# Kernel tuning notes

Hardware: AMD Instinct MI355X
Metric: run time of the kernel (lower is better)

Reference implementation:

```python
import jax, jax.numpy as jnp
import numpy as np

N_USERS = 100000
N_ENTITIES = 150000
N_RELATIONS = 10
CHANNEL = 64
N_KG_EDGES = 1000000
N_UI_EDGES = 1000000
N_HOPS = 2


def setup_inputs() -> dict:
    key = jax.random.key(0)
    ks = jax.random.split(key, 9)
    user_emb = jax.random.normal(ks[0], (N_USERS, CHANNEL), dtype=jnp.float32)
    entity_emb = jax.random.normal(ks[1], (N_ENTITIES, CHANNEL), dtype=jnp.float32)
    edge_index = jax.random.randint(ks[2], (2, N_KG_EDGES), 0, N_ENTITIES, dtype=jnp.int32)
    # edge_type in [1, n_relations) as in the repo (relation 0 is the interact relation)
    edge_type = jax.random.randint(ks[3], (N_KG_EDGES,), 1, N_RELATIONS, dtype=jnp.int32)
    ui_u = jax.random.randint(ks[4], (N_UI_EDGES,), 0, N_USERS, dtype=jnp.int32)
    ui_i = jax.random.randint(ks[5], (N_UI_EDGES,), 0, N_ENTITIES, dtype=jnp.int32)
    inter_edge = jnp.stack([ui_u, ui_i], axis=0)
    inter_edge_w = jax.random.uniform(ks[6], (N_UI_EDGES,), dtype=jnp.float32)
    # learned params (xavier_uniform)
    def xavier(k, shape):
        fan_in, fan_out = shape[0], shape[1]
        a = float(np.sqrt(6.0 / (fan_in + fan_out)))
        return jax.random.uniform(k, shape, dtype=jnp.float32, minval=-a, maxval=a)
    relation_emb = xavier(ks[7], (N_RELATIONS, CHANNEL))
    W_Q = xavier(ks[8], (CHANNEL, CHANNEL))
    W_UI = xavier(jax.random.fold_in(key, 123), (CHANNEL, CHANNEL))
    return {
        'user_emb': user_emb, 'entity_emb': entity_emb,
        'edge_index': edge_index, 'edge_type': edge_type,
        'inter_edge': inter_edge, 'inter_edge_w': inter_edge_w,
        'relation_emb': relation_emb, 'W_Q': W_Q, 'W_UI': W_UI,
    }


def _segment_softmax(score, idx, num_segments):
    # scatter_softmax: stable softmax over edges sharing the same destination index
    m = jax.ops.segment_max(score, idx, num_segments=num_segments)
    m = jnp.where(jnp.isfinite(m), m, 0.0)  # empty segments -> -inf guard
    e = jnp.exp(score - jax.lax.stop_gradient(m)[idx])
    s = jax.ops.segment_sum(e, idx, num_segments=num_segments)
    return e / (s[idx] + 1e-16)


def _l2_normalize(x):
    # F.normalize(x) with default p=2, dim=1, eps=1e-12
    n = jnp.sqrt(jnp.sum(x * x, axis=1, keepdims=True))
    return x / jnp.maximum(n, 1e-12)


def _shared_layer_agg(user_emb, entity_emb, edge_index, edge_type,
                      inter_edge, inter_edge_w, relation_emb, W_Q, W_UI):
    n_entities = entity_emb.shape[0]
    n_users = user_emb.shape[0]
    head, tail = edge_index[0], edge_index[1]
    rel = relation_emb[edge_type - 1]              # [E, C]
    query = (entity_emb[head] @ W_Q) * rel          # [E, C]
    key = (entity_emb[tail] @ W_Q) * rel            # [E, C]
    edge_attn_score = jnp.sum(query + key, axis=-1)  # [E]
    value = entity_emb[tail] * rel                  # [E, C]
    attn = _segment_softmax(edge_attn_score, head, n_entities)
    entity_agg = jax.ops.segment_sum(value * attn[:, None], head, num_segments=n_entities)
    # user-item attention; note: original code reassigns relation_emb to the per-edge
    # gathered array, so relation_emb[-1] is the relation emb of the LAST KG edge.
    rel_last = rel[-1]                              # [C]
    u_idx, i_idx = inter_edge[0], inter_edge[1]
    quary_u = (user_emb[u_idx] @ W_UI) * rel_last   # [Eui, C]
    key_i = (entity_emb[i_idx] @ W_UI) * rel_last   # [Eui, C]
    score_ui = jnp.sum(quary_u + key_i, axis=-1)
    attn_ui = _segment_softmax(score_ui, u_idx, n_users)
    item_agg = inter_edge_w[:, None] * entity_emb[i_idx] * attn_ui[:, None]
    user_agg = jax.ops.segment_sum(item_agg, u_idx, num_segments=n_users)
    return entity_agg, user_agg


def reference(user_emb, entity_emb, edge_index, edge_type, inter_edge,
              inter_edge_w, relation_emb, W_Q, W_UI):
    entity_res_emb = entity_emb
    user_res_emb = user_emb
    for _ in range(N_HOPS):
        entity_emb, user_emb = _shared_layer_agg(
            user_emb, entity_emb, edge_index, edge_type,
            inter_edge, inter_edge_w, relation_emb, W_Q, W_UI)
        # mess_dropout disabled for deterministic reference (eval mode)
        entity_emb = _l2_normalize(entity_emb)
        user_emb = _l2_normalize(user_emb)
        entity_res_emb = entity_res_emb + entity_emb
        user_res_emb = user_res_emb + user_emb
    return entity_res_emb, user_res_emb
```

## Files before the change

kernel.cpp:

```cpp
#include <hip/hip_runtime.h>


__device__ __forceinline__ float red16(float p) {
    p += __shfl_xor(p, 1, 64);
    p += __shfl_xor(p, 2, 64);
    p += __shfl_xor(p, 4, 64);
    p += __shfl_xor(p, 8, 64);
    return p;
}

__device__ __forceinline__ float bf2f(unsigned short v) {
    return __uint_as_float(((unsigned int)v) << 16);
}
__device__ __forceinline__ unsigned short f2bf(float f) {
    unsigned int u = __float_as_uint(f);
    u = (u + 0x7FFFu + ((u >> 16) & 1u)) >> 16;
    return (unsigned short)u;
}

__device__ __forceinline__ void kgfma(float4& a, float wj, ushort4 u, float4 v) {
    a.x = fmaf(wj, bf2f(u.x) * v.x, a.x);
    a.y = fmaf(wj, bf2f(u.y) * v.y, a.y);
    a.z = fmaf(wj, bf2f(u.z) * v.z, a.z);
    a.w = fmaf(wj, bf2f(u.w) * v.w, a.w);
}
__device__ __forceinline__ void uifma(float4& a, float wj, ushort4 u) {
    a.x = fmaf(wj, bf2f(u.x), a.x);
    a.y = fmaf(wj, bf2f(u.y), a.y);
    a.z = fmaf(wj, bf2f(u.z), a.z);
    a.w = fmaf(wj, bf2f(u.w), a.w);
}


__global__ void setup_kernel(const float* __restrict__ WQ,
                             const float* __restrict__ WUI,
                             const float* __restrict__ relemb,
                             const int* __restrict__ etype, int Ekg,
                             float* __restrict__ w_all,
                             const int* __restrict__ head,
                             unsigned int* __restrict__ deg_ent,
                             unsigned int* __restrict__ rank_e,
                             const int* __restrict__ uu, int Eui,
                             unsigned int* __restrict__ deg_usr,
                             unsigned int* __restrict__ rank_u) {
    if (blockIdx.x == 0) {
        for (int tid = threadIdx.x; tid < 640; tid += blockDim.x) {
            int r = tid >> 6, k = tid & 63;
            const float* M = (r == 9) ? WUI : WQ;
            int rr = (r == 9) ? (etype[Ekg - 1] - 1) : r;
            float acc = 0.f;
#pragma unroll
            for (int c = 0; c < 64; ++c)
                acc = fmaf(M[k * 64 + c], relemb[rr * 64 + c], acc);
            w_all[r * 64 + k] = acc;
        }
        return;
    }
    int e = (blockIdx.x - 1) * blockDim.x + threadIdx.x;
    if (e < Ekg) {
        rank_e[e] = atomicAdd(&deg_ent[head[e]], 1u);
    } else if (e < Ekg + Eui) {
        int e2 = e - Ekg;
        rank_u[e2] = atomicAdd(&deg_usr[uu[e2]], 1u);
    }
}


#define SCAN_CHUNK 2048

__device__ __forceinline__ void scan1_body(const unsigned int* deg, int n,
                                           unsigned int* bsums, int blk) {
    int base = blk * SCAN_CHUNK;
    int tid = threadIdx.x;
    unsigned int s = 0;
#pragma unroll
    for (int j = 0; j < 8; ++j) {
        int i = base + tid * 8 + j;
        if (i < n) s += deg[i];
    }
#pragma unroll
    for (int off = 32; off > 0; off >>= 1)
        s += __shfl_xor(s, off, 64);
    __shared__ unsigned int wsm[4];
    if ((tid & 63) == 0) wsm[tid >> 6] = s;
    __syncthreads();
    if (tid == 0) bsums[blk] = wsm[0] + wsm[1] + wsm[2] + wsm[3];
}

__global__ void scan_pass1(const unsigned int* __restrict__ dega, int na, int nba,
                           unsigned int* __restrict__ bsa,
                           const unsigned int* __restrict__ degb, int nb_,
                           unsigned int* __restrict__ bsb) {
    if ((int)blockIdx.x < nba) scan1_body(dega, na, bsa, blockIdx.x);
    else scan1_body(degb, nb_, bsb, blockIdx.x - nba);
}

__device__ __forceinline__ void scan2_body(unsigned int* bsums, int nb) {
    __shared__ unsigned int tmp[1024];
    int tid = threadIdx.x;
    unsigned int v = (tid < nb) ? bsums[tid] : 0u;
    tmp[tid] = v;
    __syncthreads();
    for (int s = 1; s < 1024; s <<= 1) {
        unsigned int add = (tid >= s) ? tmp[tid - s] : 0u;
        __syncthreads();
        tmp[tid] += add;
        __syncthreads();
    }
    if (tid < nb) bsums[tid] = tmp[tid] - v;
}

__global__ void scan_pass2(unsigned int* __restrict__ bsa, int nba,
                           unsigned int* __restrict__ bsb, int nbb) {
    if (blockIdx.x == 0) scan2_body(bsa, nba);
    else scan2_body(bsb, nbb);
}

__device__ __forceinline__ void scan3_body(const unsigned int* deg, int n,
                                           const unsigned int* bsums,
                                           unsigned int* off, int blk) {
    int base = blk * SCAN_CHUNK;
    int tid = threadIdx.x;
    int lane = tid & 63, wv = tid >> 6;
    unsigned int x[8];
    unsigned int s = 0;
#pragma unroll
    for (int j = 0; j < 8; ++j) {
        int i = base + tid * 8 + j;
        x[j] = (i < n) ? deg[i] : 0u;
        s += x[j];
    }
    unsigned int sc = s;
#pragma unroll
    for (int o = 1; o < 64; o <<= 1) {
        unsigned int t = __shfl_up(sc, o, 64);
        if (lane >= o) sc += t;
    }
    __shared__ unsigned int wtot[4];
    if (lane == 63) wtot[wv] = sc;
    __syncthreads();
    unsigned int woff = 0;
    for (int w = 0; w < wv; ++w) woff += wtot[w];
    unsigned int run = bsums[blk] + woff + (sc - s);
#pragma unroll
    for (int j = 0; j < 8; ++j) {
        int i = base + tid * 8 + j;
        run += x[j];
        if (i < n) off[i + 1] = run;
    }
    if (blk == 0 && tid == 0) off[0] = 0;
}

__global__ void scan_pass3(const unsigned int* __restrict__ dega, int na, int nba,
                           const unsigned int* __restrict__ bsa,
                           unsigned int* __restrict__ offa,
                           const unsigned int* __restrict__ degb, int nb_,
                           const unsigned int* __restrict__ bsb,
                           unsigned int* __restrict__ offb) {
    if ((int)blockIdx.x < nba) scan3_body(dega, na, bsa, offa, blockIdx.x);
    else scan3_body(degb, nb_, bsb, offb, blockIdx.x - nba);
}


__global__ void scatter_tables_kernel(
    const int* __restrict__ head, const int* __restrict__ tail,
    const int* __restrict__ etype, int Ekg,
    const unsigned int* __restrict__ off_e,
    const unsigned int* __restrict__ rank_e,
    unsigned int* __restrict__ packed,
    const int* __restrict__ uu, const int* __restrict__ ii,
    const float* __restrict__ iw, int Eui,
    const unsigned int* __restrict__ off_u,
    const unsigned int* __restrict__ rank_u,
    unsigned long long* __restrict__ sorted_iw,
    int nsc,
    const float* __restrict__ E, int n_ent, int nbe,
    const float* __restrict__ U, int n_usr,
    const float* __restrict__ w_all,
    float* __restrict__ S, float* __restrict__ su,
    unsigned short* __restrict__ Ebf) {
    if ((int)blockIdx.x < nsc) {
        int e = blockIdx.x * blockDim.x + threadIdx.x;
        if (e < Ekg) {
            int h = head[e];
            unsigned int pos = off_e[h] + rank_e[e];
            packed[pos] = (unsigned int)tail[e] |
                          (((unsigned int)(etype[e] - 1)) << 20);
        } else if (e < Ekg + Eui) {
            int e2 = e - Ekg;
            int u = uu[e2];
            unsigned int pos = off_u[u] + rank_u[e2];
            sorted_iw[pos] =
                ((unsigned long long)__float_as_uint(iw[e2]) << 32) |
                (unsigned int)ii[e2];
        }
        return;
    }
    __shared__ float4 w4[160];
    for (int i = threadIdx.x; i < 160; i += blockDim.x)
        w4[i] = ((const float4*)w_all)[i];
    __syncthreads();
    int l16 = threadIdx.x & 15;
    int bb = blockIdx.x - nsc;
    if (bb < nbe) {
        int row = bb * 16 + (threadIdx.x >> 4);
        float4 ev = make_float4(0.f, 0.f, 0.f, 0.f);
        if (row < n_ent) {
            ev = ((const float4*)E)[(size_t)row * 16 + l16];
            ushort4 eb;
            eb.x = f2bf(ev.x); eb.y = f2bf(ev.y);
            eb.z = f2bf(ev.z); eb.w = f2bf(ev.w);
            ((ushort4*)Ebf)[(size_t)row * 16 + l16] = eb;
        }
#pragma unroll
        for (int r = 0; r < 10; ++r) {
            float4 wv = w4[r * 16 + l16];
            float p = ev.x * wv.x + ev.y * wv.y + ev.z * wv.z + ev.w * wv.w;
            p = red16(p);
            if (l16 == 0 && row < n_ent) S[(size_t)row * 10 + r] = p;
        }
    } else {
        int row = (bb - nbe) * 16 + (threadIdx.x >> 4);
        float4 ev = make_float4(0.f, 0.f, 0.f, 0.f);
        if (row < n_usr) ev = ((const float4*)U)[(size_t)row * 16 + l16];
        float4 wv = w4[144 + l16];
        float p = ev.x * wv.x + ev.y * wv.y + ev.z * wv.z + ev.w * wv.w;
        p = red16(p);
        if (l16 == 0 && row < n_usr) su[row] = p;
    }
}


__global__ void hop_fused_kernel(
    const unsigned int* __restrict__ off_e,
    const unsigned int* __restrict__ packed,
    const float* __restrict__ S,
    const float* __restrict__ relemb,
    int n_ent, int nbe,
    unsigned short* __restrict__ eagg_bf, float* __restrict__ Snext,
    float* __restrict__ res_e, const float* __restrict__ res_init_e,
    const unsigned int* __restrict__ off_u,
    const unsigned long long* __restrict__ sorted_iw,
    const float* __restrict__ su, int n_usr,
    float* __restrict__ sunext,
    float* __restrict__ res_u, const float* __restrict__ res_init_u,
    const unsigned short* __restrict__ Ebf,
    const float* __restrict__ w_all) {
    __shared__ float4 rel4[144];
    __shared__ float4 w4[160];
    for (int i = threadIdx.x; i < 144; i += blockDim.x)
        rel4[i] = ((const float4*)relemb)[i];
    for (int i = threadIdx.x; i < 160; i += blockDim.x)
        w4[i] = ((const float4*)w_all)[i];
    __syncthreads();

    int lane = threadIdx.x & 63;
    int l16 = lane & 15;
    int gbase = lane & 48;

    if ((int)blockIdx.x < nbe) {
        int h = blockIdx.x * 16 + (threadIdx.x >> 4);
        if (h >= n_ent) return;
        unsigned int s0 = off_e[h], s1 = off_e[h + 1];
        float shv = (l16 < 10) ? S[(size_t)h * 10 + l16] : 0.f;

        float4 a0 = make_float4(0.f, 0.f, 0.f, 0.f);
        float4 a1 = make_float4(0.f, 0.f, 0.f, 0.f);
        float4 a2 = make_float4(0.f, 0.f, 0.f, 0.f);
        float4 a3 = make_float4(0.f, 0.f, 0.f, 0.f);
        float wsum = 0.f;
        for (unsigned int base = s0; base < s1; base += 16) {
            unsigned int rem = s1 - base;
            unsigned int c = rem < 16u ? rem : 16u;
            unsigned int pk = (l16 < (int)c) ? packed[base + l16] : 0u;
            int t = pk & 0xFFFFF, r = pk >> 20;
            float st = S[(size_t)t * 10 + r];
            float q = __shfl(shv, gbase + r, 64);
            float wg = (l16 < (int)c) ? __expf(q + st) : 0.f;
            wsum += red16(wg);
            unsigned int j = 0;
            for (; j + 4 <= c; j += 4) {
                unsigned int p0 = (unsigned int)__shfl((int)pk, gbase + (int)j, 64);
                unsigned int p1 = (unsigned int)__shfl((int)pk, gbase + (int)j + 1, 64);
                unsigned int p2 = (unsigned int)__shfl((int)pk, gbase + (int)j + 2, 64);
                unsigned int p3 = (unsigned int)__shfl((int)pk, gbase + (int)j + 3, 64);
                float w0 = __shfl(wg, gbase + (int)j, 64);
                float w1 = __shfl(wg, gbase + (int)j + 1, 64);
                float w2 = __shfl(wg, gbase + (int)j + 2, 64);
                float w3 = __shfl(wg, gbase + (int)j + 3, 64);
                int t0 = p0 & 0xFFFFF, t1 = p1 & 0xFFFFF;
                int t2 = p2 & 0xFFFFF, t3 = p3 & 0xFFFFF;
                ushort4 u0 = ((const ushort4*)Ebf)[(size_t)t0 * 16 + l16];
                ushort4 u1 = ((const ushort4*)Ebf)[(size_t)t1 * 16 + l16];
                ushort4 u2 = ((const ushort4*)Ebf)[(size_t)t2 * 16 + l16];
                ushort4 u3 = ((const ushort4*)Ebf)[(size_t)t3 * 16 + l16];
                kgfma(a0, w0, u0, rel4[(p0 >> 20) * 16 + l16]);
                kgfma(a1, w1, u1, rel4[(p1 >> 20) * 16 + l16]);
                kgfma(a2, w2, u2, rel4[(p2 >> 20) * 16 + l16]);
                kgfma(a3, w3, u3, rel4[(p3 >> 20) * 16 + l16]);
            }
            for (; j < c; ++j) {
                unsigned int p0 = (unsigned int)__shfl((int)pk, gbase + (int)j, 64);
                float w0 = __shfl(wg, gbase + (int)j, 64);
                int t0 = p0 & 0xFFFFF;
                ushort4 u0 = ((const ushort4*)Ebf)[(size_t)t0 * 16 + l16];
                kgfma(a0, w0, u0, rel4[(p0 >> 20) * 16 + l16]);
            }
        }
        float4 acc = make_float4(a0.x + a1.x + a2.x + a3.x,
                                 a0.y + a1.y + a2.y + a3.y,
                                 a0.z + a1.z + a2.z + a3.z,
                                 a0.w + a1.w + a2.w + a3.w);
        float inv = 1.f / (wsum + 1e-16f);
        float4 y = make_float4(acc.x * inv, acc.y * inv, acc.z * inv, acc.w * inv);
        float ss = red16(y.x * y.x + y.y * y.y + y.z * y.z + y.w * y.w);
        float sinv = 1.f / fmaxf(sqrtf(ss), 1e-12f);
        y.x *= sinv; y.y *= sinv; y.z *= sinv; y.w *= sinv;

        size_t ro = (size_t)h * 16 + l16;
        if (eagg_bf) {
            ushort4 yb;
            yb.x = f2bf(y.x); yb.y = f2bf(y.y);
            yb.z = f2bf(y.z); yb.w = f2bf(y.w);
            ((ushort4*)eagg_bf)[ro] = yb;
        }
        float4 b4 = res_init_e ? ((const float4*)res_init_e)[ro]
                               : ((const float4*)res_e)[ro];
        ((float4*)res_e)[ro] = make_float4(b4.x + y.x, b4.y + y.y,
                                           b4.z + y.z, b4.w + y.w);
        if (Snext) {
#pragma unroll
            for (int r2 = 0; r2 < 10; ++r2) {
                float4 wv = w4[r2 * 16 + l16];
                float p = red16(y.x * wv.x + y.y * wv.y + y.z * wv.z + y.w * wv.w);
                if (l16 == 0) Snext[(size_t)h * 10 + r2] = p;
            }
        }
    } else {
        int u = (blockIdx.x - nbe) * 16 + (threadIdx.x >> 4);
        if (u >= n_usr) return;
        unsigned int s0 = off_u[u], s1 = off_u[u + 1];
        float squ = su[u];

        float4 a0 = make_float4(0.f, 0.f, 0.f, 0.f);
        float4 a1 = make_float4(0.f, 0.f, 0.f, 0.f);
        float4 a2 = make_float4(0.f, 0.f, 0.f, 0.f);
        float4 a3 = make_float4(0.f, 0.f, 0.f, 0.f);
        float wsum = 0.f;
        for (unsigned int base = s0; base < s1; base += 16) {
            unsigned int rem = s1 - base;
            unsigned int c = rem < 16u ? rem : 16u;
            unsigned int iv = 0; float wg = 0.f, cw = 0.f;
            if (l16 < (int)c) {
                unsigned long long t8 = sorted_iw[base + l16];
                iv = (unsigned int)t8;
                float sw = __uint_as_float((unsigned int)(t8 >> 32));
                wg = __expf(squ + S[(size_t)iv * 10 + 9]);
                cw = wg * sw;
            }
            wsum += red16(wg);
            unsigned int j = 0;
            for (; j + 4 <= c; j += 4) {
                unsigned int i0 = (unsigned int)__shfl((int)iv, gbase + (int)j, 64);
                unsigned int i1 = (unsigned int)__shfl((int)iv, gbase + (int)j + 1, 64);
                unsigned int i2 = (unsigned int)__shfl((int)iv, gbase + (int)j + 2, 64);
                unsigned int i3 = (unsigned int)__shfl((int)iv, gbase + (int)j + 3, 64);
                float w0 = __shfl(cw, gbase + (int)j, 64);
                float w1 = __shfl(cw, gbase + (int)j + 1, 64);
                float w2 = __shfl(cw, gbase + (int)j + 2, 64);
                float w3 = __shfl(cw, gbase + (int)j + 3, 64);
                ushort4 u0 = ((const ushort4*)Ebf)[(size_t)i0 * 16 + l16];
                ushort4 u1 = ((const ushort4*)Ebf)[(size_t)i1 * 16 + l16];
                ushort4 u2 = ((const ushort4*)Ebf)[(size_t)i2 * 16 + l16];
                ushort4 u3 = ((const ushort4*)Ebf)[(size_t)i3 * 16 + l16];
                uifma(a0, w0, u0);
                uifma(a1, w1, u1);
                uifma(a2, w2, u2);
                uifma(a3, w3, u3);
            }
            for (; j < c; ++j) {
                unsigned int i0 = (unsigned int)__shfl((int)iv, gbase + (int)j, 64);
                float w0 = __shfl(cw, gbase + (int)j, 64);
                ushort4 u0 = ((const ushort4*)Ebf)[(size_t)i0 * 16 + l16];
                uifma(a0, w0, u0);
            }
        }
        float4 acc = make_float4(a0.x + a1.x + a2.x + a3.x,
                                 a0.y + a1.y + a2.y + a3.y,
                                 a0.z + a1.z + a2.z + a3.z,
                                 a0.w + a1.w + a2.w + a3.w);
        float inv = 1.f / (wsum + 1e-16f);
        float4 y = make_float4(acc.x * inv, acc.y * inv, acc.z * inv, acc.w * inv);
        float ss = red16(y.x * y.x + y.y * y.y + y.z * y.z + y.w * y.w);
        float sinv = 1.f / fmaxf(sqrtf(ss), 1e-12f);
        y.x *= sinv; y.y *= sinv; y.z *= sinv; y.w *= sinv;

        size_t ro = (size_t)u * 16 + l16;
        float4 b4 = res_init_u ? ((const float4*)res_init_u)[ro]
                               : ((const float4*)res_u)[ro];
        ((float4*)res_u)[ro] = make_float4(b4.x + y.x, b4.y + y.y,
                                           b4.z + y.z, b4.w + y.w);
        if (sunext) {
            float4 wv = w4[144 + l16];
            float p = red16(y.x * wv.x + y.y * wv.y + y.z * wv.z + y.w * wv.w);
            if (l16 == 0) sunext[u] = p;
        }
    }
}


extern "C" void kernel_launch(void* const* d_in, const int* in_sizes, int n_in,
                              void* d_out, int out_size, void* d_ws, size_t ws_size,
                              hipStream_t stream) {
    const float* user_emb   = (const float*)d_in[0];
    const float* entity_emb = (const float*)d_in[1];
    const int*   edge_index = (const int*)d_in[2];
    const int*   edge_type  = (const int*)d_in[3];
    const int*   inter_edge = (const int*)d_in[4];
    const float* inter_w    = (const float*)d_in[5];
    const float* relemb     = (const float*)d_in[6];
    const float* WQ         = (const float*)d_in[7];
    const float* WUI        = (const float*)d_in[8];

    const int C = 64;
    const int n_usr = in_sizes[0] / C;
    const int n_ent = in_sizes[1] / C;
    const int Ekg   = in_sizes[3];
    const int Eui   = in_sizes[5];
    const int* head = edge_index;
    const int* tail = edge_index + Ekg;
    const int* uu   = inter_edge;
    const int* ii   = inter_edge + Eui;

    float* ws = (float*)d_ws;
    float* w_all = ws;                          ws += 640;
    float* S0    = ws;                          ws += (size_t)n_ent * 10;
    float* S1    = ws;                          ws += (size_t)n_ent * 10;
    float* su0   = ws;                          ws += n_usr;
    float* su1   = ws;                          ws += n_usr;
    unsigned int* deg_ent = (unsigned int*)ws;  ws += n_ent;
    unsigned int* deg_usr = (unsigned int*)ws;  ws += n_usr;
    unsigned int* off_ent = (unsigned int*)ws;  ws += n_ent + 1;
    unsigned int* off_usr = (unsigned int*)ws;  ws += n_usr + 1;
    unsigned int* bsum_e  = (unsigned int*)ws;  ws += 1024;
    unsigned int* bsum_u  = (unsigned int*)ws;  ws += 1024;
    unsigned int* rank_e  = (unsigned int*)ws;  ws += Ekg;
    unsigned int* rank_u  = (unsigned int*)ws;  ws += Eui;
    unsigned int* packed  = (unsigned int*)ws;  ws += Ekg;

    uintptr_t p16 = ((uintptr_t)ws + 15) & ~(uintptr_t)15;
    unsigned long long* sorted_iw = (unsigned long long*)p16;
    p16 += (size_t)Eui * 8;
    unsigned short* ebf0 = (unsigned short*)p16;
    p16 += (size_t)n_ent * 64 * 2;
    unsigned short* ebf1 = (unsigned short*)p16;

    float* out_ent = (float*)d_out;
    float* out_usr = out_ent + (size_t)n_ent * C;

    hipMemsetAsync(deg_ent, 0, (size_t)(n_ent + n_usr) * sizeof(unsigned int), stream);
    setup_kernel<<<1 + (Ekg + Eui + 255) / 256, 256, 0, stream>>>(
        WQ, WUI, relemb, edge_type, Ekg, w_all,
        head, deg_ent, rank_e, uu, Eui, deg_usr, rank_u);

    int nb_e = (n_ent + SCAN_CHUNK - 1) / SCAN_CHUNK;
    int nb_u = (n_usr + SCAN_CHUNK - 1) / SCAN_CHUNK;
    scan_pass1<<<nb_e + nb_u, 256, 0, stream>>>(deg_ent, n_ent, nb_e, bsum_e,
                                                deg_usr, n_usr, bsum_u);
    scan_pass2<<<2, 1024, 0, stream>>>(bsum_e, nb_e, bsum_u, nb_u);
    scan_pass3<<<nb_e + nb_u, 256, 0, stream>>>(deg_ent, n_ent, nb_e, bsum_e, off_ent,
                                                deg_usr, n_usr, bsum_u, off_usr);

    int nsc = (Ekg + Eui + 255) / 256;
    int nbe = (n_ent + 15) / 16;
    int nbu = (n_usr + 15) / 16;
    scatter_tables_kernel<<<nsc + nbe + nbu, 256, 0, stream>>>(
        head, tail, edge_type, Ekg, off_ent, rank_e, packed,
        uu, ii, inter_w, Eui, off_usr, rank_u, sorted_iw, nsc,
        entity_emb, n_ent, nbe, user_emb, n_usr, w_all, S0, su0, ebf0);

    hop_fused_kernel<<<nbe + nbu, 256, 0, stream>>>(
        off_ent, packed, S0, relemb, n_ent, nbe,
        ebf1, S1, out_ent, entity_emb,
        off_usr, sorted_iw, su0, n_usr,
        su1, out_usr, user_emb,
        ebf0, w_all);

    hop_fused_kernel<<<nbe + nbu, 256, 0, stream>>>(
        off_ent, packed, S1, relemb, n_ent, nbe,
        nullptr, nullptr, out_ent, nullptr,
        off_usr, sorted_iw, su1, n_usr,
        nullptr, out_usr, nullptr,
        ebf1, w_all);
}
```

Baseline: 389.8 us.

## Recompute attention scores from gathered bf16 rows instead of gathering precomputed S

The KG and UI aggregation loops no longer gather a precomputed per-entity score from S. Each gathered bf16 embedding row is instead dotted with the relation-specific W vector in LDS and reduced across 16 lanes, which drops one scattered 4-byte load per edge. In exchange, every edge now pays a 16-lane shuffle reduction, and the inner unroll shrinks from 4 to 2, which reduces the number of gathers in flight. The recomputed score uses bf16-rounded embeddings, which may slightly change numerics.

```diff
diff --git a/kernel.cpp b/kernel.cpp
--- a/kernel.cpp
+++ b/kernel.cpp
@@ -17,18 +17,23 @@
     u = (u + 0x7FFFu + ((u >> 16) & 1u)) >> 16;
     return (unsigned short)u;
 }
-
-__device__ __forceinline__ void kgfma(float4& a, float wj, ushort4 u, float4 v) {
-    a.x = fmaf(wj, bf2f(u.x) * v.x, a.x);
-    a.y = fmaf(wj, bf2f(u.y) * v.y, a.y);
-    a.z = fmaf(wj, bf2f(u.z) * v.z, a.z);
-    a.w = fmaf(wj, bf2f(u.w) * v.w, a.w);
-}
-__device__ __forceinline__ void uifma(float4& a, float wj, ushort4 u) {
-    a.x = fmaf(wj, bf2f(u.x), a.x);
-    a.y = fmaf(wj, bf2f(u.y), a.y);
-    a.z = fmaf(wj, bf2f(u.z), a.z);
-    a.w = fmaf(wj, bf2f(u.w), a.w);
+__device__ __forceinline__ float4 bfx4(ushort4 u) {
+    return make_float4(bf2f(u.x), bf2f(u.y), bf2f(u.z), bf2f(u.w));
+}
+__device__ __forceinline__ float dot4(float4 a, float4 b) {
+    return a.x * b.x + a.y * b.y + a.z * b.z + a.w * b.w;
+}
+__device__ __forceinline__ void fma4r(float4& a, float w, float4 f, float4 v) {
+    a.x = fmaf(w, f.x * v.x, a.x);
+    a.y = fmaf(w, f.y * v.y, a.y);
+    a.z = fmaf(w, f.z * v.z, a.z);
+    a.w = fmaf(w, f.w * v.w, a.w);
+}
+__device__ __forceinline__ void fma4(float4& a, float w, float4 f) {
+    a.x = fmaf(w, f.x, a.x);
+    a.y = fmaf(w, f.y, a.y);
+    a.z = fmaf(w, f.z, a.z);
+    a.w = fmaf(w, f.w, a.w);
 }
 
 
@@ -215,17 +220,14 @@
 #pragma unroll
         for (int r = 0; r < 10; ++r) {
             float4 wv = w4[r * 16 + l16];
-            float p = ev.x * wv.x + ev.y * wv.y + ev.z * wv.z + ev.w * wv.w;
-            p = red16(p);
+            float p = red16(dot4(ev, wv));
             if (l16 == 0 && row < n_ent) S[(size_t)row * 10 + r] = p;
         }
     } else {
         int row = (bb - nbe) * 16 + (threadIdx.x >> 4);
         float4 ev = make_float4(0.f, 0.f, 0.f, 0.f);
         if (row < n_usr) ev = ((const float4*)U)[(size_t)row * 16 + l16];
-        float4 wv = w4[144 + l16];
-        float p = ev.x * wv.x + ev.y * wv.y + ev.z * wv.z + ev.w * wv.w;
-        p = red16(p);
+        float p = red16(dot4(ev, w4[144 + l16]));
         if (l16 == 0 && row < n_usr) su[row] = p;
     }
 }
@@ -266,54 +268,45 @@
 
         float4 a0 = make_float4(0.f, 0.f, 0.f, 0.f);
         float4 a1 = make_float4(0.f, 0.f, 0.f, 0.f);
-        float4 a2 = make_float4(0.f, 0.f, 0.f, 0.f);
-        float4 a3 = make_float4(0.f, 0.f, 0.f, 0.f);
         float wsum = 0.f;
         for (unsigned int base = s0; base < s1; base += 16) {
             unsigned int rem = s1 - base;
             unsigned int c = rem < 16u ? rem : 16u;
             unsigned int pk = (l16 < (int)c) ? packed[base + l16] : 0u;
-            int t = pk & 0xFFFFF, r = pk >> 20;
-            float st = S[(size_t)t * 10 + r];
-            float q = __shfl(shv, gbase + r, 64);
-            float wg = (l16 < (int)c) ? __expf(q + st) : 0.f;
-            wsum += red16(wg);
             unsigned int j = 0;
-            for (; j + 4 <= c; j += 4) {
+            for (; j + 2 <= c; j += 2) {
                 unsigned int p0 = (unsigned int)__shfl((int)pk, gbase + (int)j, 64);
                 unsigned int p1 = (unsigned int)__shfl((int)pk, gbase + (int)j + 1, 64);
-                unsigned int p2 = (unsigned int)__shfl((int)pk, gbase + (int)j + 2, 64);
-                unsigned int p3 = (unsigned int)__shfl((int)pk, gbase + (int)j + 3, 64);
-                float w0 = __shfl(wg, gbase + (int)j, 64);
-                float w1 = __shfl(wg, gbase + (int)j + 1, 64);
-                float w2 = __shfl(wg, gbase + (int)j + 2, 64);
-                float w3 = __shfl(wg, gbase + (int)j + 3, 64);
-                int t0 = p0 & 0xFFFFF, t1 = p1 & 0xFFFFF;
-                int t2 = p2 & 0xFFFFF, t3 = p3 & 0xFFFFF;
-                ushort4 u0 = ((const ushort4*)Ebf)[(size_t)t0 * 16 + l16];
-                ushort4 u1 = ((const ushort4*)Ebf)[(size_t)t1 * 16 + l16];
-                ushort4 u2 = ((const ushort4*)Ebf)[(size_t)t2 * 16 + l16];
-                ushort4 u3 = ((const ushort4*)Ebf)[(size_t)t3 * 16 + l16];
-                kgfma(a0, w0, u0, rel4[(p0 >> 20) * 16 + l16]);
-                kgfma(a1, w1, u1, rel4[(p1 >> 20) * 16 + l16]);
-                kgfma(a2, w2, u2, rel4[(p2 >> 20) * 16 + l16]);
-                kgfma(a3, w3, u3, rel4[(p3 >> 20) * 16 + l16]);
+                int t0 = p0 & 0xFFFFF, r0 = p0 >> 20;
+                int t1 = p1 & 0xFFFFF, r1 = p1 >> 20;
+                float4 f0 = bfx4(((const ushort4*)Ebf)[(size_t)t0 * 16 + l16]);
+                float4 f1 = bfx4(((const ushort4*)Ebf)[(size_t)t1 * 16 + l16]);
+                float d0 = red16(dot4(f0, w4[r0 * 16 + l16]));
+                float d1 = red16(dot4(f1, w4[r1 * 16 + l16]));
+                float q0 = __shfl(shv, gbase + r0, 64);
+                float q1 = __shfl(shv, gbase + r1, 64);
+                float wg0 = __expf(q0 + d0);
+                float wg1 = __expf(q1 + d1);
+                wsum += wg0 + wg1;
+                fma4r(a0, wg0, f0, rel4[r0 * 16 + l16]);
+                fma4r(a1, wg1, f1, rel4[r1 * 16 + l16]);
             }
-            for (; j < c; ++j) {
+            if (j < c) {
                 unsigned int p0 = (unsigned int)__shfl((int)pk, gbase + (int)j, 64);
-                float w0 = __shfl(wg, gbase + (int)j, 64);
-                int t0 = p0 & 0xFFFFF;
-                ushort4 u0 = ((const ushort4*)Ebf)[(size_t)t0 * 16 + l16];
-                kgfma(a0, w0, u0, rel4[(p0 >> 20) * 16 + l16]);
+                int t0 = p0 & 0xFFFFF, r0 = p0 >> 20;
+                float4 f0 = bfx4(((const ushort4*)Ebf)[(size_t)t0 * 16 + l16]);
+                float d0 = red16(dot4(f0, w4[r0 * 16 + l16]));
+                float q0 = __shfl(shv, gbase + r0, 64);
+                float wg0 = __expf(q0 + d0);
+                wsum += wg0;
+                fma4r(a0, wg0, f0, rel4[r0 * 16 + l16]);
             }
         }
-        float4 acc = make_float4(a0.x + a1.x + a2.x + a3.x,
-                                 a0.y + a1.y + a2.y + a3.y,
-                                 a0.z + a1.z + a2.z + a3.z,
-                                 a0.w + a1.w + a2.w + a3.w);
+        float4 acc = make_float4(a0.x + a1.x, a0.y + a1.y,
+                                 a0.z + a1.z, a0.w + a1.w);
         float inv = 1.f / (wsum + 1e-16f);
         float4 y = make_float4(acc.x * inv, acc.y * inv, acc.z * inv, acc.w * inv);
-        float ss = red16(y.x * y.x + y.y * y.y + y.z * y.z + y.w * y.w);
+        float ss = red16(dot4(y, y));
         float sinv = 1.f / fmaxf(sqrtf(ss), 1e-12f);
         y.x *= sinv; y.y *= sinv; y.z *= sinv; y.w *= sinv;
 
@@ -331,8 +324,7 @@
         if (Snext) {
 #pragma unroll
             for (int r2 = 0; r2 < 10; ++r2) {
-                float4 wv = w4[r2 * 16 + l16];
-                float p = red16(y.x * wv.x + y.y * wv.y + y.z * wv.z + y.w * wv.w);
+                float p = red16(dot4(y, w4[r2 * 16 + l16]));
                 if (l16 == 0) Snext[(size_t)h * 10 + r2] = p;
             }
         }
@@ -341,57 +333,48 @@
         if (u >= n_usr) return;
         unsigned int s0 = off_u[u], s1 = off_u[u + 1];
         float squ = su[u];
+        float4 w9v = w4[144 + l16];
 
         float4 a0 = make_float4(0.f, 0.f, 0.f, 0.f);
         float4 a1 = make_float4(0.f, 0.f, 0.f, 0.f);
-        float4 a2 = make_float4(0.f, 0.f, 0.f, 0.f);
-        float4 a3 = make_float4(0.f, 0.f, 0.f, 0.f);
         float wsum = 0.f;
         for (unsigned int base = s0; base < s1; base += 16) {
             unsigned int rem = s1 - base;
             unsigned int c = rem < 16u ? rem : 16u;
-            unsigned int iv = 0; float wg = 0.f, cw = 0.f;
-            if (l16 < (int)c) {
-                unsigned long long t8 = sorted_iw[base + l16];
-                iv = (unsigned int)t8;
-                float sw = __uint_as_float((unsigned int)(t8 >> 32));
-                wg = __expf(squ + S[(size_t)iv * 10 + 9]);
-                cw = wg * sw;
-            }
-            wsum += red16(wg);
+            unsigned long long t8 = (l16 < (int)c) ? sorted_iw[base + l16] : 0ull;
+            unsigned int iv = (unsigned int)t8;
+            float sw = __uint_as_float((unsigned int)(t8 >> 32));
             unsigned int j = 0;
-            for (; j + 4 <= c; j += 4) {
+            for (; j + 2 <= c; j += 2) {
                 unsigned int i0 = (unsigned int)__shfl((int)iv, gbase + (int)j, 64);
                 unsigned int i1 = (unsigned int)__shfl((int)iv, gbase + (int)j + 1, 64);
-                unsigned int i2 = (unsigned int)__shfl((int)iv, gbase + (int)j + 2, 64);
-                unsigned int i3 = (unsigned int)__shfl((int)iv, gbase + (int)j + 3, 64);
-                float w0 = __shfl(cw, gbase + (int)j, 64);
-                float w1 = __shfl(cw, gbase + (int)j + 1, 64);
-                float w2 = __shfl(cw, gbase + (int)j + 2, 64);
-                float w3 = __shfl(cw, gbase + (int)j + 3, 64);
-                ushort4 u0 = ((const ushort4*)Ebf)[(size_t)i0 * 16 + l16];
-                ushort4 u1 = ((const ushort4*)Ebf)[(size_t)i1 * 16 + l16];
-                ushort4 u2 = ((const ushort4*)Ebf)[(size_t)i2 * 16 + l16];
-                ushort4 u3 = ((const ushort4*)Ebf)[(size_t)i3 * 16 + l16];
-                uifma(a0, w0, u0);
-                uifma(a1, w1, u1);
-                uifma(a2, w2, u2);
-                uifma(a3, w3, u3);
+                float sw0 = __shfl(sw, gbase + (int)j, 64);
+                float sw1 = __shfl(sw, gbase + (int)j + 1, 64);
+                float4 f0 = bfx4(((const ushort4*)Ebf)[(size_t)i0 * 16 + l16]);
+                float4 f1 = bfx4(((const ushort4*)Ebf)[(size_t)i1 * 16 + l16]);
+                float d0 = red16(dot4(f0, w9v));
+                float d1 = red16(dot4(f1, w9v));
+                float wg0 = __expf(squ + d0);
+                float wg1 = __expf(squ + d1);
+                wsum += wg0 + wg1;
+                fma4(a0, wg0 * sw0, f0);
+                fma4(a1, wg1 * sw1, f1);
             }
-            for (; j < c; ++j) {
+            if (j < c) {
                 unsigned int i0 = (unsigned int)__shfl((int)iv, gbase + (int)j, 64);
-                float w0 = __shfl(cw, gbase + (int)j, 64);
-                ushort4 u0 = ((const ushort4*)Ebf)[(size_t)i0 * 16 + l16];
-                uifma(a0, w0, u0);
+                float sw0 = __shfl(sw, gbase + (int)j, 64);
+                float4 f0 = bfx4(((const ushort4*)Ebf)[(size_t)i0 * 16 + l16]);
+                float d0 = red16(dot4(f0, w9v));
+                float wg0 = __expf(squ + d0);
+                wsum += wg0;
+                fma4(a0, wg0 * sw0, f0);
             }
         }
-        float4 acc = make_float4(a0.x + a1.x + a2.x + a3.x,
-                                 a0.y + a1.y + a2.y + a3.y,
-                                 a0.z + a1.z + a2.z + a3.z,
-                                 a0.w + a1.w + a2.w + a3.w);
+        float4 acc = make_float4(a0.x + a1.x, a0.y + a1.y,
+                                 a0.z + a1.z, a0.w + a1.w);
         float inv = 1.f / (wsum + 1e-16f);
         float4 y = make_float4(acc.x * inv, acc.y * inv, acc.z * inv, acc.w * inv);
-        float ss = red16(y.x * y.x + y.y * y.y + y.z * y.z + y.w * y.w);
+        float ss = red16(dot4(y, y));
         float sinv = 1.f / fmaxf(sqrtf(ss), 1e-12f);
         y.x *= sinv; y.y *= sinv; y.z *= sinv; y.w *= sinv;
 
@@ -401,8 +384,7 @@
         ((float4*)res_u)[ro] = make_float4(b4.x + y.x, b4.y + y.y,
                                            b4.z + y.z, b4.w + y.w);
         if (sunext) {
-            float4 wv = w4[144 + l16];
-            float p = red16(y.x * wv.x + y.y * wv.y + y.z * wv.z + y.w * wv.w);
+            float p = red16(dot4(y, w9v));
             if (l16 == 0) sunext[u] = p;
         }
     }
```

Result: faster. 328.0 us (-15.9%).
